# Kernel tuning notes

Hardware: AMD Instinct MI355X
Metric: run time of the kernel (lower is better)

The kernel has to match this reference:

```python
import jax, jax.numpy as jnp
import numpy as np


def _span_indices(seq_len: int, max_width: int):
    # static index construction (mirrors the torch loop over windows/positions)
    starts, ends, wids = [], [], []
    for w in range(1, max_width + 1):
        n = seq_len - w + 1
        s = np.arange(n, dtype=np.int32)
        starts.append(s)
        ends.append(s + w - 1)
        wids.append(np.full(n, w - 1, dtype=np.int32))
    return (np.concatenate(starts), np.concatenate(ends), np.concatenate(wids))


def setup_inputs() -> dict:
    key = jax.random.key(0)
    k1, k2 = jax.random.split(key)
    B, L, D = 16, 512, 768
    W, WD = 8, 64  # span_maximum_length, span_width_embedding_dim
    x = jax.random.normal(k1, (B, L, D), dtype=jnp.float32)
    width_emb = jax.random.normal(k2, (W, WD), dtype=jnp.float32)
    return {"x": x, "width_emb": width_emb, "batch_max_seq_len": L}


def reference(x, width_emb, batch_max_seq_len):
    # x: [B, L, D]; width_emb: [max_width, WD]
    B = x.shape[0]
    max_width = min(batch_max_seq_len, width_emb.shape[0])
    starts, ends, wids = _span_indices(batch_max_seq_len, max_width)
    starts = jnp.asarray(starts)
    ends = jnp.asarray(ends)
    wids = jnp.asarray(wids)
    n_spans = starts.shape[0]
    h_start = x[:, starts, :]                     # [B, n_spans, D]
    h_end = x[:, ends, :]                         # [B, n_spans, D]
    w_feat = jnp.broadcast_to(width_emb[wids][None, :, :],
                              (B, n_spans, width_emb.shape[1]))
    # si,j = [h_i; h_j; f_width(i,j)] -> [B, n_spans, 2D + WD]
    return jnp.concatenate([h_start, h_end, w_feat], axis=-1)
```

## Files before the change

kernel.cpp:

```cpp
#include <hip/hip_runtime.h>

typedef float f32x4 __attribute__((ext_vector_type(4)));

constexpr uint32_t B  = 16;
constexpr uint32_t L  = 512;
constexpr uint32_t D4 = 768 / 4;
constexpr uint32_t WD4 = 64 / 4;
constexpr uint32_t NSPANS = 4068;
constexpr uint32_t ROW_F4 = 2 * D4 + WD4;
constexpr uint32_t TOTAL_F4 = B * NSPANS * ROW_F4;

constexpr uint32_t TPB = 256;
constexpr uint32_t F4_PER_THREAD = 8;
constexpr uint32_t CHUNK = TPB * F4_PER_THREAD;

__global__ __launch_bounds__(TPB) void span_rep_kernel(
    const f32x4* __restrict__ x4,
    const f32x4* __restrict__ w4,
    f32x4* __restrict__ out4) {
  uint32_t idx = blockIdx.x * CHUNK + threadIdx.x;
  if (idx >= TOTAL_F4) return;

  uint32_t r = idx / ROW_F4;
  uint32_t c = idx - r * ROW_F4;
  uint32_t b = r / NSPANS;
  uint32_t s = r - b * NSPANS;

  uint32_t wid = 0;
#pragma unroll
  for (uint32_t k = 1; k < 8; ++k) {
    const uint32_t o = L * k - (k * (k - 1)) / 2;
    wid += (s >= o) ? 1u : 0u;
  }
  uint32_t off   = L * wid - (wid * (wid - 1u)) / 2u;
  uint32_t start = s - off;

#pragma unroll
  for (uint32_t i = 0; i < F4_PER_THREAD; ++i) {
    if (idx < TOTAL_F4) {
      f32x4 v;
      if (c < D4) {
        v = x4[(b * L + start) * D4 + c];
      } else if (c < 2 * D4) {
        v = x4[(b * L + start + wid) * D4 + (c - D4)];
      } else {
        v = w4[wid * WD4 + (c - 2 * D4)];
      }
      __builtin_nontemporal_store(v, &out4[idx]);
    }
    idx += TPB;
    c   += TPB;
    if (c >= ROW_F4) {
      c -= ROW_F4;
      ++start;
      ++s;
      if (s == NSPANS) {
        ++b; s = 0; wid = 0; start = 0;
      } else if (start == L - wid) {
        ++wid; start = 0;
      }
    }
  }
}

extern "C" void kernel_launch(void* const* d_in, const int* in_sizes, int n_in,
                              void* d_out, int out_size, void* d_ws, size_t ws_size,
                              hipStream_t stream) {
  const f32x4* x4 = (const f32x4*)d_in[0];
  const f32x4* w4 = (const f32x4*)d_in[1];
  f32x4* out4 = (f32x4*)d_out;

  uint32_t blocks = (TOTAL_F4 + CHUNK - 1u) / CHUNK;
  span_rep_kernel<<<dim3(blocks), dim3(TPB), 0, stream>>>(x4, w4, out4);
}
```

Baseline: 434.1 us.

## Use grid-stride loop with fixed column per thread and batched loads

Replaces the per-block contiguous chunk with a fixed grid of blocks striding over the output by a multiple of the row width. Each thread keeps a constant column, so the branch selecting x-start, x-end or width embedding is hoisted out of the loop. Four loads are issued before their four nontemporal stores to raise memory-level parallelism. The exact-cover static asserts tie the grid size to the problem shape, and fewer blocks may reduce occupancy-driven latency hiding.

```diff
diff --git a/kernel.cpp b/kernel.cpp
--- a/kernel.cpp
+++ b/kernel.cpp
@@ -2,64 +2,75 @@
 
 typedef float f32x4 __attribute__((ext_vector_type(4)));
 
-constexpr uint32_t B  = 16;
-constexpr uint32_t L  = 512;
-constexpr uint32_t D4 = 768 / 4;
-constexpr uint32_t WD4 = 64 / 4;
+constexpr uint32_t B      = 16;
+constexpr uint32_t L      = 512;
+constexpr uint32_t D4     = 768 / 4;
+constexpr uint32_t WD4    = 64 / 4;
 constexpr uint32_t NSPANS = 4068;
 constexpr uint32_t ROW_F4 = 2 * D4 + WD4;
 constexpr uint32_t TOTAL_F4 = B * NSPANS * ROW_F4;
 
-constexpr uint32_t TPB = 256;
-constexpr uint32_t F4_PER_THREAD = 8;
-constexpr uint32_t CHUNK = TPB * F4_PER_THREAD;
+constexpr uint32_t TPB  = 256;
+constexpr uint32_t NBLK = 2825;
+constexpr uint32_t T    = TPB * NBLK;
+constexpr uint32_t NITER = TOTAL_F4 / T;
+static_assert(NITER * T == TOTAL_F4, "exact cover");
+static_assert(T % ROW_F4 == 0, "c invariant");
+constexpr uint32_t DS = T / ROW_F4;
+constexpr uint32_t XB_STRIDE = L * D4;
+constexpr uint32_t U = 4;
 
 __global__ __launch_bounds__(TPB) void span_rep_kernel(
     const f32x4* __restrict__ x4,
     const f32x4* __restrict__ w4,
     f32x4* __restrict__ out4) {
-  uint32_t idx = blockIdx.x * CHUNK + threadIdx.x;
-  if (idx >= TOTAL_F4) return;
+  uint32_t idx = blockIdx.x * TPB + threadIdx.x;
 
+  const uint32_t c = idx % ROW_F4;
   uint32_t r = idx / ROW_F4;
-  uint32_t c = idx - r * ROW_F4;
-  uint32_t b = r / NSPANS;
-  uint32_t s = r - b * NSPANS;
+  uint32_t s  = r;
+  uint32_t xb = 0;
 
-  uint32_t wid = 0;
-#pragma unroll
-  for (uint32_t k = 1; k < 8; ++k) {
-    const uint32_t o = L * k - (k * (k - 1)) / 2;
-    wid += (s >= o) ? 1u : 0u;
-  }
-  uint32_t off   = L * wid - (wid * (wid - 1u)) / 2u;
-  uint32_t start = s - off;
+  const bool     isW   = c >= 2 * D4;
+  const bool     isMid = (c >= D4) && !isW;
+  const uint32_t c2    = isW ? 0u : (isMid ? c - D4 : c);
+  const uint32_t cw    = isW ? c - 2 * D4 : 0u;
+
+  for (uint32_t it = 0; it < NITER / U; ++it) {
+    const f32x4* pv[U];
+    uint32_t so[U];
 
 #pragma unroll
-  for (uint32_t i = 0; i < F4_PER_THREAD; ++i) {
-    if (idx < TOTAL_F4) {
-      f32x4 v;
-      if (c < D4) {
-        v = x4[(b * L + start) * D4 + c];
-      } else if (c < 2 * D4) {
-        v = x4[(b * L + start + wid) * D4 + (c - D4)];
-      } else {
-        v = w4[wid * WD4 + (c - 2 * D4)];
+    for (uint32_t u = 0; u < U; ++u) {
+      uint32_t wid = 0;
+#pragma unroll
+      for (uint32_t k = 1; k < 8; ++k) {
+        const uint32_t o = L * k - (k * (k - 1)) / 2;
+        wid += (s >= o) ? 1u : 0u;
       }
-      __builtin_nontemporal_store(v, &out4[idx]);
+      const uint32_t off   = (wid * (2u * L + 1u - wid)) >> 1;
+      const uint32_t start = s - off;
+      const uint32_t row   = start + (isMid ? wid : 0u);
+
+      const f32x4* px = x4 + (xb + row * D4 + c2);
+      const f32x4* pw = w4 + (wid * WD4 + cw);
+      pv[u] = isW ? pw : px;
+      so[u] = idx;
+
+      idx += T;
+      s   += DS;
+      const bool wrap = s >= NSPANS;
+      s  -= wrap ? NSPANS : 0u;
+      xb += wrap ? XB_STRIDE : 0u;
     }
-    idx += TPB;
-    c   += TPB;
-    if (c >= ROW_F4) {
-      c -= ROW_F4;
-      ++start;
-      ++s;
-      if (s == NSPANS) {
-        ++b; s = 0; wid = 0; start = 0;
-      } else if (start == L - wid) {
-        ++wid; start = 0;
-      }
-    }
+
+    f32x4 v[U];
+#pragma unroll
+    for (uint32_t u = 0; u < U; ++u) v[u] = *pv[u];
+
+#pragma unroll
+    for (uint32_t u = 0; u < U; ++u)
+      __builtin_nontemporal_store(v[u], &out4[so[u]]);
   }
 }
 
@@ -69,7 +80,5 @@
   const f32x4* x4 = (const f32x4*)d_in[0];
   const f32x4* w4 = (const f32x4*)d_in[1];
   f32x4* out4 = (f32x4*)d_out;
-
-  uint32_t blocks = (TOTAL_F4 + CHUNK - 1u) / CHUNK;
-  span_rep_kernel<<<dim3(blocks), dim3(TPB), 0, stream>>>(x4, w4, out4);
+  span_rep_kernel<<<dim3(NBLK), dim3(TPB), 0, stream>>>(x4, w4, out4);
 }
```

Measured after the change: 450.0 us. 3.7% more time.

## Remap blocks to per-batch start-position buckets looping over span widths

Applied to the files above, without the earlier changes.

Each block now owns a batch and a bucket of 8 start positions, and loops over all 8 span widths, writing the contiguous output rows for each width. This keeps the same input rows hot in cache across widths and removes the per-element division and width search. In exchange the grid shrinks to 1024 blocks with long per-thread loops, which may reduce occupancy and the parallelism available to saturate write bandwidth.

```diff
diff --git a/kernel.cpp b/kernel.cpp
--- a/kernel.cpp
+++ b/kernel.cpp
@@ -2,64 +2,54 @@
 
 typedef float f32x4 __attribute__((ext_vector_type(4)));
 
-constexpr uint32_t B  = 16;
-constexpr uint32_t L  = 512;
-constexpr uint32_t D4 = 768 / 4;
-constexpr uint32_t WD4 = 64 / 4;
+constexpr uint32_t B      = 16;
+constexpr uint32_t L      = 512;
+constexpr uint32_t D4     = 768 / 4;
+constexpr uint32_t WD4    = 64 / 4;
 constexpr uint32_t NSPANS = 4068;
 constexpr uint32_t ROW_F4 = 2 * D4 + WD4;
-constexpr uint32_t TOTAL_F4 = B * NSPANS * ROW_F4;
 
-constexpr uint32_t TPB = 256;
-constexpr uint32_t F4_PER_THREAD = 8;
-constexpr uint32_t CHUNK = TPB * F4_PER_THREAD;
+constexpr uint32_t P    = 8;
+constexpr uint32_t NPB  = L / P;
+constexpr uint32_t TPB  = 256;
+constexpr uint32_t BUCKET_F4 = P * ROW_F4;
+constexpr uint32_t ITERS = (BUCKET_F4 + TPB - 1) / TPB;
 
 __global__ __launch_bounds__(TPB) void span_rep_kernel(
     const f32x4* __restrict__ x4,
     const f32x4* __restrict__ w4,
     f32x4* __restrict__ out4) {
-  uint32_t idx = blockIdx.x * CHUNK + threadIdx.x;
-  if (idx >= TOTAL_F4) return;
+  const uint32_t bid = blockIdx.x;
+  const uint32_t b   = bid >> 6;
+  const uint32_t p0  = (bid & 63u) * P;
+  const uint32_t t   = threadIdx.x;
+  const uint32_t xb  = b * (L * D4);
 
-  uint32_t r = idx / ROW_F4;
-  uint32_t c = idx - r * ROW_F4;
-  uint32_t b = r / NSPANS;
-  uint32_t s = r - b * NSPANS;
-
-  uint32_t wid = 0;
-#pragma unroll
-  for (uint32_t k = 1; k < 8; ++k) {
-    const uint32_t o = L * k - (k * (k - 1)) / 2;
-    wid += (s >= o) ? 1u : 0u;
-  }
-  uint32_t off   = L * wid - (wid * (wid - 1u)) / 2u;
-  uint32_t start = s - off;
+  uint32_t ok = 0;
+  for (uint32_t k = 0; k < 8; ++k) {
+    const uint32_t nspan = min(P, L - k - p0);
+    const uint32_t nval  = nspan * ROW_F4;
+    const uint32_t obase = (b * NSPANS + ok + p0) * ROW_F4;
 
 #pragma unroll
-  for (uint32_t i = 0; i < F4_PER_THREAD; ++i) {
-    if (idx < TOTAL_F4) {
-      f32x4 v;
-      if (c < D4) {
-        v = x4[(b * L + start) * D4 + c];
-      } else if (c < 2 * D4) {
-        v = x4[(b * L + start + wid) * D4 + (c - D4)];
-      } else {
-        v = w4[wid * WD4 + (c - 2 * D4)];
-      }
-      __builtin_nontemporal_store(v, &out4[idx]);
-    }
-    idx += TPB;
-    c   += TPB;
-    if (c >= ROW_F4) {
-      c -= ROW_F4;
-      ++start;
-      ++s;
-      if (s == NSPANS) {
-        ++b; s = 0; wid = 0; start = 0;
-      } else if (start == L - wid) {
-        ++wid; start = 0;
+    for (uint32_t it = 0; it < ITERS; ++it) {
+      const uint32_t e = it * TPB + t;
+      if (e < nval) {
+        const uint32_t p   = e / ROW_F4;
+        const uint32_t c   = e - p * ROW_F4;
+        const uint32_t row = p0 + p;
+        f32x4 v;
+        if (c < D4) {
+          v = x4[xb + row * D4 + c];
+        } else if (c < 2 * D4) {
+          v = x4[xb + (row + k) * D4 + (c - D4)];
+        } else {
+          v = w4[k * WD4 + (c - 2 * D4)];
+        }
+        __builtin_nontemporal_store(v, &out4[obase + e]);
       }
     }
+    ok += L - k;
   }
 }
 
@@ -69,7 +59,5 @@
   const f32x4* x4 = (const f32x4*)d_in[0];
   const f32x4* w4 = (const f32x4*)d_in[1];
   f32x4* out4 = (f32x4*)d_out;
-
-  uint32_t blocks = (TOTAL_F4 + CHUNK - 1u) / CHUNK;
-  span_rep_kernel<<<dim3(blocks), dim3(TPB), 0, stream>>>(x4, w4, out4);
+  span_rep_kernel<<<dim3(B * NPB), dim3(TPB), 0, stream>>>(x4, w4, out4);
 }
```

Result: no change. 437.0 us (+0.7%).
